# Optimization experiments

Hardware: AMD Instinct MI355X
Metric: run time of the kernel (lower is better)

Reference implementation:

```python
import jax, jax.numpy as jnp
import numpy as np

REG_MAX = 16
NC = 80
STRIDES = (8, 16, 32)
IMGSZ = 640
MAX_DETS = 300
CONF = 0.25


def setup_inputs() -> dict:
    key = jax.random.key(0)
    k1, k2, k3 = jax.random.split(key, 3)
    B, C = 64, 4 * REG_MAX + NC
    return {
        "p8": jax.random.normal(k1, (B, C, 80, 80), dtype=jnp.float32),
        "p16": jax.random.normal(k2, (B, C, 40, 40), dtype=jnp.float32),
        "p32": jax.random.normal(k3, (B, C, 20, 20), dtype=jnp.float32),
    }


def _make_anchors(shapes, strides, dtype):
    anc, st = [], []
    for (h, w), s in zip(shapes, strides):
        sx = jnp.arange(w, dtype=dtype) + 0.5
        sy = jnp.arange(h, dtype=dtype) + 0.5
        yy, xx = jnp.meshgrid(sy, sx, indexing="ij")
        anc.append(jnp.stack([xx, yy], axis=-1).reshape(-1, 2))  # [h*w, 2]
        st.append(jnp.full((h * w,), float(s), dtype=dtype))
    anc_points = jnp.concatenate(anc, axis=0).T[None]  # [1, 2, A]
    stride_t = jnp.concatenate(st, axis=0)[None]       # [1, A]
    return anc_points, stride_t


def _forward(p8, p16, p32):
    preds = [p8, p16, p32]
    dtype = p8.dtype
    b = p8.shape[0]
    shapes = [(p.shape[2], p.shape[3]) for p in preds]
    anc_points, stride_t = _make_anchors(shapes, STRIDES, dtype)

    idx = jnp.arange(REG_MAX, dtype=dtype).reshape(1, 1, REG_MAX, 1)
    dists, clss = [], []
    for p in preds:
        _, c, h, w = p.shape
        a = h * w
        p = p.reshape(b, c, a)
        box = p[:, : 4 * REG_MAX].reshape(b, 4, REG_MAX, a)
        probs = jax.nn.softmax(box, axis=2)
        dists.append(jnp.sum(probs * idx, axis=2))  # [b, 4, a]
        clss.append(p[:, 4 * REG_MAX :])             # [b, nc, a]
    dist_all = jnp.concatenate(dists, axis=2)        # [b, 4, A]
    cls_all = jax.nn.sigmoid(jnp.concatenate(clss, axis=2))  # [b, nc, A]

    # dist2bbox (xyxy): x1y1 = anchor - lt, x2y2 = anchor + rb
    lt, rb = dist_all[:, :2], dist_all[:, 2:]
    dbox = jnp.concatenate([anc_points - lt, anc_points + rb], axis=1) * stride_t[:, None, :]
    boxes = jnp.transpose(dbox, (0, 2, 1))           # [b, A, 4]
    scores = jnp.transpose(cls_all, (0, 2, 1))       # [b, A, nc]

    best_scores = jnp.max(scores, axis=2)            # [b, A]
    best_cls = jnp.argmax(scores, axis=2)            # [b, A]
    masked = jnp.where(best_scores >= CONF, best_scores, jnp.full_like(best_scores, -1.0))
    k = min(MAX_DETS, masked.shape[1])
    _, top_idx = jax.lax.top_k(masked, k)            # [b, k]

    sel_boxes = jnp.take_along_axis(boxes, top_idx[..., None], axis=1)  # [b, k, 4]
    sel_scores = jnp.take_along_axis(best_scores, top_idx, axis=1)      # [b, k]
    sel_cls = jnp.take_along_axis(best_cls, top_idx, axis=1).astype(dtype)

    lim = jnp.asarray(IMGSZ, dtype)
    sel_boxes = jnp.clip(sel_boxes, 0.0, lim)
    sel_scores = jnp.maximum(sel_scores, 0.0)
    detections = jnp.concatenate(
        [sel_boxes, sel_scores[..., None], sel_cls[..., None]], axis=-1
    )  # [b, k, 6]
    num_dets = jnp.sum(sel_scores >= CONF, axis=1).astype(jnp.int32)
    return detections, num_dets


def reference(p8, p16, p32):
    return _forward(p8, p16, p32)
```

## Files before the change

kernel.cpp:

```cpp
#include <hip/hip_runtime.h>
#include <stdint.h>

#define RMAX   16
#define NCLS   80
#define NCH    144
#define A8     6400
#define ATOT   8400
#define KDET   300
#define NBATCH 64
#define CONF_T 0.25f
#define IMG_F  640.0f

__device__ __forceinline__ uint32_t desc_key(float f) {
    uint32_t u = __float_as_uint(f);
    uint32_t m = (u & 0x80000000u) ? ~u : (u | 0x80000000u);
    return ~m;
}

__global__ __launch_bounds__(256, 6) void decode_kernel(
    const float* __restrict__ p8, const float* __restrict__ p16,
    const float* __restrict__ p32,
    float4* __restrict__ boxes, float* __restrict__ score,
    float* __restrict__ cls, uint32_t* __restrict__ ord)
{
    const int a = blockIdx.x * 256 + threadIdx.x;
    if (a >= ATOT) return;
    const int b = blockIdx.y;

    const float* p; int HW, W, pix; float strideS;
    if (a < A8)        { p = p8;  HW = 6400; W = 80; pix = a;        strideS = 8.f;  }
    else if (a < 8000) { p = p16; HW = 1600; W = 40; pix = a - 6400; strideS = 16.f; }
    else               { p = p32; HW = 400;  W = 20; pix = a - 8000; strideS = 32.f; }

    const int y = pix / W;
    const int x = pix - y * W;
    const float* base = p + (size_t)b * NCH * HW + pix;

    float dist[4];
#pragma unroll
    for (int j = 0; j < 4; ++j) {
        float v[16];
#pragma unroll
        for (int i = 0; i < 16; ++i) v[i] = base[(size_t)(j * 16 + i) * HW];
        float mx = v[0];
#pragma unroll
        for (int i = 1; i < 16; ++i) mx = fmaxf(mx, v[i]);
        float s = 0.f, wsum = 0.f;
#pragma unroll
        for (int i = 0; i < 16; ++i) {
            float e = __expf(v[i] - mx);
            s += e; wsum += e * (float)i;
        }
        dist[j] = wsum / s;
    }

    float ml = -3.402823466e38f; int am = 0;
#pragma unroll 8
    for (int c = 0; c < NCLS; ++c) {
        float t = base[(size_t)(64 + c) * HW];
        if (t > ml) { ml = t; am = c; }
    }

    const size_t gi = (size_t)b * ATOT + a;
    const float ax = (float)x + 0.5f, ay = (float)y + 0.5f;
    float4 bx;
    bx.x = (ax - dist[0]) * strideS;
    bx.y = (ay - dist[1]) * strideS;
    bx.z = (ax + dist[2]) * strideS;
    bx.w = (ay + dist[3]) * strideS;
    boxes[gi] = bx;
    const float sc = 1.0f / (1.0f + __expf(-ml));
    score[gi] = sc;
    cls[gi] = (float)am;
    ord[gi] = (sc >= CONF_T) ? desc_key(ml) : 0xFFFFFFFFu;
}

__device__ __forceinline__ int block_reduce_sum(int v, volatile int* red) {
    const int tid = threadIdx.x;
    red[tid] = v;
    __syncthreads();
    for (int s = 128; s > 0; s >>= 1) {
        if (tid < s) red[tid] += red[tid + s];
        __syncthreads();
    }
    int r = red[0];
    __syncthreads();
    return r;
}

__global__ __launch_bounds__(256) void topk_kernel(
    const float4* __restrict__ boxes, const float* __restrict__ score,
    const float* __restrict__ clsArr, const uint32_t* __restrict__ ordArr,
    float* __restrict__ out)
{
    __shared__ uint32_t sk[ATOT];
    __shared__ int hist[256];
    __shared__ int scanb[256];
    __shared__ int red[256];
    __shared__ unsigned long long win[KDET];
    __shared__ int eqIdx[64];
    __shared__ int s_digit, s_m, eqCnt, cnt, ndet;
    const int tid = threadIdx.x;
    const int b = blockIdx.x;

    for (int i = tid; i < ATOT; i += 256) sk[i] = ordArr[(size_t)b * ATOT + i];
    if (tid == 0) { eqCnt = 0; cnt = 0; ndet = 0; }
    __syncthreads();

    uint32_t prefix = 0; int m = KDET;
#pragma unroll
    for (int pass = 3; pass >= 0; --pass) {
        const uint32_t hiMask = (pass == 3) ? 0u : (0xFFFFFFFFu << ((pass + 1) * 8));
        const int sh = pass * 8;
        hist[tid] = 0;
        __syncthreads();
        for (int i = tid; i < ATOT; i += 256) {
            const uint32_t k = sk[i];
            if (((k ^ prefix) & hiMask) == 0)
                atomicAdd(&hist[(k >> sh) & 0xFF], 1);
        }
        __syncthreads();
        scanb[tid] = hist[tid];
        __syncthreads();
        for (int off = 1; off < 256; off <<= 1) {
            const int t = (tid >= off) ? scanb[tid - off] : 0;
            __syncthreads();
            scanb[tid] += t;
            __syncthreads();
        }
        const int prev = (tid == 0) ? 0 : scanb[tid - 1];
        if (scanb[tid] >= m && prev < m) { s_digit = tid; s_m = m - prev; }
        __syncthreads();
        prefix |= ((uint32_t)s_digit) << sh;
        m = s_m;
    }
    const uint32_t T = prefix;

    for (int i = tid; i < ATOT; i += 256) {
        if (sk[i] == T) { const int p = atomicAdd(&eqCnt, 1); if (p < 64) eqIdx[p] = i; }
    }
    __syncthreads();
    const int ec = eqCnt;

    for (int i = tid; i < ATOT; i += 256) {
        const uint32_t k = sk[i];
        if (k < T) { const int p = atomicAdd(&cnt, 1); win[p] = ((unsigned long long)k << 32) | (uint32_t)i; }
    }
    if (ec <= 64) {
        if (tid < ec) {
            const int my = eqIdx[tid]; int r = 0;
            for (int v2 = 0; v2 < ec; ++v2) r += (eqIdx[v2] < my) ? 1 : 0;
            if (r < m) { const int p = atomicAdd(&cnt, 1); win[p] = ((unsigned long long)T << 32) | (uint32_t)my; }
        }
    } else {
        int ilo = 0, ihi = ATOT - 1;
        while (ilo < ihi) {
            const int mid = (ilo + ihi) >> 1;
            int cc = 0;
            for (int i = tid; i <= mid; i += 256) cc += (sk[i] == T) ? 1 : 0;
            cc = block_reduce_sum(cc, red);
            if (cc >= m) ihi = mid; else ilo = mid + 1;
        }
        for (int i = tid; i <= ilo; i += 256) {
            if (sk[i] == T) { const int p = atomicAdd(&cnt, 1); win[p] = ((unsigned long long)T << 32) | (uint32_t)i; }
        }
    }
    __syncthreads();

    int local_nd = 0;
    for (int w = tid; w < KDET; w += 256) {
        const unsigned long long k = win[w];
        int r = 0;
        for (int v2 = 0; v2 < KDET; ++v2) r += (win[v2] < k) ? 1 : 0;
        const uint32_t a = (uint32_t)(k & 0xFFFFFFFFu);
        const size_t gi = (size_t)b * ATOT + a;
        const float4 bx = boxes[gi];
        const float sc = fmaxf(score[gi], 0.0f);
        const float cl = clsArr[gi];
        float* row = out + ((size_t)b * KDET + r) * 6;
        row[0] = fminf(fmaxf(bx.x, 0.0f), IMG_F);
        row[1] = fminf(fmaxf(bx.y, 0.0f), IMG_F);
        row[2] = fminf(fmaxf(bx.z, 0.0f), IMG_F);
        row[3] = fminf(fmaxf(bx.w, 0.0f), IMG_F);
        row[4] = sc;
        row[5] = cl;
        if (sc >= CONF_T) ++local_nd;
    }
    atomicAdd(&ndet, local_nd);
    __syncthreads();
    if (tid == 0) out[(size_t)NBATCH * KDET * 6 + b] = (float)ndet;
}

extern "C" void kernel_launch(void* const* d_in, const int* in_sizes, int n_in,
                              void* d_out, int out_size, void* d_ws, size_t ws_size,
                              hipStream_t stream) {
    const float* p8  = (const float*)d_in[0];
    const float* p16 = (const float*)d_in[1];
    const float* p32 = (const float*)d_in[2];

    char* ws = (char*)d_ws;
    const size_t nBA = (size_t)NBATCH * ATOT;
    float4*   boxes  = (float4*)ws;
    float*    score  = (float*)(ws + 16 * nBA);
    float*    cls    = (float*)(ws + 20 * nBA);
    uint32_t* ord    = (uint32_t*)(ws + 24 * nBA);

    decode_kernel<<<dim3(33, NBATCH), dim3(256), 0, stream>>>(
        p8, p16, p32, boxes, score, cls, ord);

    topk_kernel<<<dim3(NBATCH), dim3(256), 0, stream>>>(
        boxes, score, cls, ord, (float*)d_out);
}
```

Measured before the change: 430.3 us.

## Stage decode tiles via global_load_lds, split work across waves, bisect topk threshold

The decode kernel now handles 64 anchors per block. It stages all 144 channels into LDS with direct global-to-LDS 16-byte loads, and the four waves each take one box side plus a quarter of the classes, combining partial argmax results through shared memory. The topk kernel replaces the four-pass radix histogram with its atomics and scans by a 32-step binary search on the threshold key, using wave shuffles for the reductions. The aim is better memory-level parallelism in decode and fewer barriers and atomics in topk. In exchange, decode uses more LDS per block and its final stage runs on a single wave, and the search makes 32 full passes over the keys in shared memory.

```diff
diff --git a/kernel.cpp b/kernel.cpp
--- a/kernel.cpp
+++ b/kernel.cpp
@@ -4,7 +4,6 @@
 #define RMAX   16
 #define NCLS   80
 #define NCH    144
-#define A8     6400
 #define ATOT   8400
 #define KDET   300
 #define NBATCH 64
@@ -17,31 +16,46 @@
     return ~m;
 }
 
-__global__ __launch_bounds__(256, 6) void decode_kernel(
+__global__ __launch_bounds__(256) void decode_kernel(
     const float* __restrict__ p8, const float* __restrict__ p16,
     const float* __restrict__ p32,
     float4* __restrict__ boxes, float* __restrict__ score,
     float* __restrict__ cls, uint32_t* __restrict__ ord)
 {
-    const int a = blockIdx.x * 256 + threadIdx.x;
-    if (a >= ATOT) return;
-    const int b = blockIdx.y;
-
-    const float* p; int HW, W, pix; float strideS;
-    if (a < A8)        { p = p8;  HW = 6400; W = 80; pix = a;        strideS = 8.f;  }
-    else if (a < 8000) { p = p16; HW = 1600; W = 40; pix = a - 6400; strideS = 16.f; }
-    else               { p = p32; HW = 400;  W = 20; pix = a - 8000; strideS = 32.f; }
-
-    const int y = pix / W;
-    const int x = pix - y * W;
-    const float* base = p + (size_t)b * NCH * HW + pix;
-
-    float dist[4];
-#pragma unroll
-    for (int j = 0; j < 4; ++j) {
+    __shared__ float tile[NCH * 64];
+    __shared__ float distS[4 * 64];
+    __shared__ float mlS[4 * 64];
+    __shared__ int   amS[4 * 64];
+
+    const int bx = blockIdx.x, b = blockIdx.y;
+    const float* p; int HW, W, local, abase, nanc; float strideS;
+    if (bx < 100)      { p = p8;  HW = 6400; W = 80; local = bx * 64;         abase = local;        nanc = 64; strideS = 8.f; }
+    else if (bx < 125) { p = p16; HW = 1600; W = 40; local = (bx - 100) * 64; abase = 6400 + local; nanc = 64; strideS = 16.f; }
+    else               { p = p32; HW = 400;  W = 20; local = (bx - 125) * 64; abase = 8000 + local;
+                         nanc = (400 - local >= 64) ? 64 : (400 - local);     strideS = 32.f; }
+
+    const int t = threadIdx.x, w = t >> 6, lane = t & 63;
+    const int vec = lane & 15, chIn = lane >> 4;
+    const int nvec = nanc >> 2;
+    const float* gb = p + (size_t)b * NCH * HW + local;
+
+#pragma unroll
+    for (int k = 0; k < 9; ++k) {
+        const int c = w + k * 4;
+        if (vec < nvec) {
+            const float* g = gb + (size_t)(c * 4 + chIn) * HW + vec * 4;
+            __builtin_amdgcn_global_load_lds(
+                (const __attribute__((address_space(1))) void*)g,
+                (__attribute__((address_space(3))) void*)(tile + c * 256),
+                16, 0, 0);
+        }
+    }
+    __syncthreads();
+
+    if (lane < nanc) {
         float v[16];
 #pragma unroll
-        for (int i = 0; i < 16; ++i) v[i] = base[(size_t)(j * 16 + i) * HW];
+        for (int i = 0; i < 16; ++i) v[i] = tile[(w * 16 + i) * 64 + lane];
         float mx = v[0];
 #pragma unroll
         for (int i = 1; i < 16; ++i) mx = fmaxf(mx, v[i]);
@@ -51,41 +65,46 @@
             float e = __expf(v[i] - mx);
             s += e; wsum += e * (float)i;
         }
-        dist[j] = wsum / s;
-    }
-
-    float ml = -3.402823466e38f; int am = 0;
-#pragma unroll 8
-    for (int c = 0; c < NCLS; ++c) {
-        float t = base[(size_t)(64 + c) * HW];
-        if (t > ml) { ml = t; am = c; }
-    }
-
-    const size_t gi = (size_t)b * ATOT + a;
-    const float ax = (float)x + 0.5f, ay = (float)y + 0.5f;
-    float4 bx;
-    bx.x = (ax - dist[0]) * strideS;
-    bx.y = (ay - dist[1]) * strideS;
-    bx.z = (ax + dist[2]) * strideS;
-    bx.w = (ay + dist[3]) * strideS;
-    boxes[gi] = bx;
-    const float sc = 1.0f / (1.0f + __expf(-ml));
-    score[gi] = sc;
-    cls[gi] = (float)am;
-    ord[gi] = (sc >= CONF_T) ? desc_key(ml) : 0xFFFFFFFFu;
-}
-
-__device__ __forceinline__ int block_reduce_sum(int v, volatile int* red) {
-    const int tid = threadIdx.x;
-    red[tid] = v;
-    __syncthreads();
-    for (int s = 128; s > 0; s >>= 1) {
-        if (tid < s) red[tid] += red[tid + s];
-        __syncthreads();
-    }
-    int r = red[0];
-    __syncthreads();
-    return r;
+        distS[w * 64 + lane] = wsum / s;
+
+        float ml = -3.402823466e38f; int am = 0;
+#pragma unroll
+        for (int c2 = 0; c2 < 20; ++c2) {
+            const float tv = tile[(64 + w * 20 + c2) * 64 + lane];
+            if (tv > ml) { ml = tv; am = w * 20 + c2; }
+        }
+        mlS[w * 64 + lane] = ml; amS[w * 64 + lane] = am;
+    }
+    __syncthreads();
+
+    if (w == 0 && lane < nanc) {
+        float ml = mlS[lane]; int am = amS[lane];
+#pragma unroll
+        for (int ww = 1; ww < 4; ++ww) {
+            const float m2 = mlS[ww * 64 + lane];
+            if (m2 > ml) { ml = m2; am = amS[ww * 64 + lane]; }
+        }
+        const int pix = local + lane;
+        const int y = pix / W, x = pix - y * W;
+        const float ax = (float)x + 0.5f, ay = (float)y + 0.5f;
+        float4 bb;
+        bb.x = (ax - distS[lane])       * strideS;
+        bb.y = (ay - distS[64 + lane])  * strideS;
+        bb.z = (ax + distS[128 + lane]) * strideS;
+        bb.w = (ay + distS[192 + lane]) * strideS;
+        const size_t gi = (size_t)b * ATOT + abase + lane;
+        boxes[gi] = bb;
+        const float sc = 1.0f / (1.0f + __expf(-ml));
+        score[gi] = sc;
+        cls[gi] = (float)am;
+        ord[gi] = (sc >= CONF_T) ? desc_key(ml) : 0xFFFFFFFFu;
+    }
+}
+
+__device__ __forceinline__ int wave_sum(int v) {
+#pragma unroll
+    for (int o = 32; o > 0; o >>= 1) v += __shfl_down(v, o, 64);
+    return v;
 }
 
 __global__ __launch_bounds__(256) void topk_kernel(
@@ -94,63 +113,57 @@
     float* __restrict__ out)
 {
     __shared__ uint32_t sk[ATOT];
-    __shared__ int hist[256];
-    __shared__ int scanb[256];
-    __shared__ int red[256];
+    __shared__ int red4[2][4];
     __shared__ unsigned long long win[KDET];
     __shared__ int eqIdx[64];
-    __shared__ int s_digit, s_m, eqCnt, cnt, ndet;
+    __shared__ int eqCnt, cnt, ndet;
     const int tid = threadIdx.x;
+    const int w = tid >> 6, lane = tid & 63;
     const int b = blockIdx.x;
 
     for (int i = tid; i < ATOT; i += 256) sk[i] = ordArr[(size_t)b * ATOT + i];
     if (tid == 0) { eqCnt = 0; cnt = 0; ndet = 0; }
     __syncthreads();
 
-    uint32_t prefix = 0; int m = KDET;
-#pragma unroll
-    for (int pass = 3; pass >= 0; --pass) {
-        const uint32_t hiMask = (pass == 3) ? 0u : (0xFFFFFFFFu << ((pass + 1) * 8));
-        const int sh = pass * 8;
-        hist[tid] = 0;
+    uint32_t lo = 0u, hi = 0xFFFFFFFFu;
+    int parity = 0;
+    while (lo < hi) {
+        const uint32_t mid = lo + ((hi - lo) >> 1);
+        int c = 0;
+        for (int i = tid; i < ATOT; i += 256) c += (sk[i] <= mid) ? 1 : 0;
+        c = wave_sum(c);
+        if (lane == 0) red4[parity][w] = c;
         __syncthreads();
-        for (int i = tid; i < ATOT; i += 256) {
-            const uint32_t k = sk[i];
-            if (((k ^ prefix) & hiMask) == 0)
-                atomicAdd(&hist[(k >> sh) & 0xFF], 1);
-        }
-        __syncthreads();
-        scanb[tid] = hist[tid];
-        __syncthreads();
-        for (int off = 1; off < 256; off <<= 1) {
-            const int t = (tid >= off) ? scanb[tid - off] : 0;
-            __syncthreads();
-            scanb[tid] += t;
-            __syncthreads();
-        }
-        const int prev = (tid == 0) ? 0 : scanb[tid - 1];
-        if (scanb[tid] >= m && prev < m) { s_digit = tid; s_m = m - prev; }
-        __syncthreads();
-        prefix |= ((uint32_t)s_digit) << sh;
-        m = s_m;
-    }
-    const uint32_t T = prefix;
+        c = red4[parity][0] + red4[parity][1] + red4[parity][2] + red4[parity][3];
+        parity ^= 1;
+        if (c >= KDET) hi = mid; else lo = mid + 1;
+    }
+    const uint32_t T = lo;
+
+    int c = 0;
+    for (int i = tid; i < ATOT; i += 256) c += (sk[i] < T) ? 1 : 0;
+    c = wave_sum(c);
+    if (lane == 0) red4[parity][w] = c;
+    __syncthreads();
+    const int c_less = red4[parity][0] + red4[parity][1] + red4[parity][2] + red4[parity][3];
+    parity ^= 1;
+    const int m = KDET - c_less;
 
     for (int i = tid; i < ATOT; i += 256) {
-        if (sk[i] == T) { const int p = atomicAdd(&eqCnt, 1); if (p < 64) eqIdx[p] = i; }
+        if (sk[i] == T) { const int p2 = atomicAdd(&eqCnt, 1); if (p2 < 64) eqIdx[p2] = i; }
     }
     __syncthreads();
     const int ec = eqCnt;
 
     for (int i = tid; i < ATOT; i += 256) {
         const uint32_t k = sk[i];
-        if (k < T) { const int p = atomicAdd(&cnt, 1); win[p] = ((unsigned long long)k << 32) | (uint32_t)i; }
+        if (k < T) { const int p2 = atomicAdd(&cnt, 1); win[p2] = ((unsigned long long)k << 32) | (uint32_t)i; }
     }
     if (ec <= 64) {
         if (tid < ec) {
             const int my = eqIdx[tid]; int r = 0;
             for (int v2 = 0; v2 < ec; ++v2) r += (eqIdx[v2] < my) ? 1 : 0;
-            if (r < m) { const int p = atomicAdd(&cnt, 1); win[p] = ((unsigned long long)T << 32) | (uint32_t)my; }
+            if (r < m) { const int p2 = atomicAdd(&cnt, 1); win[p2] = ((unsigned long long)T << 32) | (uint32_t)my; }
         }
     } else {
         int ilo = 0, ihi = ATOT - 1;
@@ -158,18 +171,22 @@
             const int mid = (ilo + ihi) >> 1;
             int cc = 0;
             for (int i = tid; i <= mid; i += 256) cc += (sk[i] == T) ? 1 : 0;
-            cc = block_reduce_sum(cc, red);
+            cc = wave_sum(cc);
+            if (lane == 0) red4[parity][w] = cc;
+            __syncthreads();
+            cc = red4[parity][0] + red4[parity][1] + red4[parity][2] + red4[parity][3];
+            parity ^= 1;
             if (cc >= m) ihi = mid; else ilo = mid + 1;
         }
         for (int i = tid; i <= ilo; i += 256) {
-            if (sk[i] == T) { const int p = atomicAdd(&cnt, 1); win[p] = ((unsigned long long)T << 32) | (uint32_t)i; }
+            if (sk[i] == T) { const int p2 = atomicAdd(&cnt, 1); win[p2] = ((unsigned long long)T << 32) | (uint32_t)i; }
         }
     }
     __syncthreads();
 
     int local_nd = 0;
-    for (int w = tid; w < KDET; w += 256) {
-        const unsigned long long k = win[w];
+    for (int ww = tid; ww < KDET; ww += 256) {
+        const unsigned long long k = win[ww];
         int r = 0;
         for (int v2 = 0; v2 < KDET; ++v2) r += (win[v2] < k) ? 1 : 0;
         const uint32_t a = (uint32_t)(k & 0xFFFFFFFFu);
@@ -205,7 +222,7 @@
     float*    cls    = (float*)(ws + 20 * nBA);
     uint32_t* ord    = (uint32_t*)(ws + 24 * nBA);
 
-    decode_kernel<<<dim3(33, NBATCH), dim3(256), 0, stream>>>(
+    decode_kernel<<<dim3(132, NBATCH), dim3(256), 0, stream>>>(
         p8, p16, p32, boxes, score, cls, ord);
 
     topk_kernel<<<dim3(NBATCH), dim3(256), 0, stream>>>(
```

Measured after the change: 406.7 us. -5.5%, faster.
